# Optimization experiments

Measured on AMD Instinct MI355X. Metric: run time of the kernel, lower is better.

The kernel has to match this reference:

```python
import jax, jax.numpy as jnp
import numpy as np

D_STATE = 8
DT_RANK = 8  # ceil(128/16)


def _grouped_1x1(x, w):
    # x: (B,H,W,Cin), w: (g, Cout//g, Cin//g)
    B, H, W, _ = x.shape
    g, o, i = w.shape
    xg = x.reshape(B, H, W, g, i)
    return jnp.einsum('bhwgi,goi->bhwgo', xg, w).reshape(B, H, W, g * o)


def setup_inputs() -> dict:
    key = jax.random.key(0)
    ks = jax.random.split(key, 16)
    B, H, W, C = 8, 64, 64, 128
    g = 4
    D = 128  # expand_dim = d_inner
    N = D_STATE
    R = DT_RANK
    inp = {}
    inp['x'] = jax.random.normal(ks[0], (B, H, W, C), dtype=jnp.float32)
    inp['w1'] = jax.random.normal(ks[1], (g, D // g, C // g), dtype=jnp.float32) * 0.1
    inp['dw'] = jax.random.normal(ks[2], (3, 3, 1, D), dtype=jnp.float32) * 0.1  # HWIO depthwise
    inp['in_proj_w'] = jax.random.normal(ks[3], (2 * D, D), dtype=jnp.float32) * 0.05
    inp['conv1d_w'] = jax.random.normal(ks[4], (D, 3), dtype=jnp.float32) * 0.1
    inp['conv1d_b'] = jax.random.normal(ks[5], (D,), dtype=jnp.float32) * 0.05
    inp['x_proj_w'] = jax.random.normal(ks[6], (R + 2 * N, D), dtype=jnp.float32) * 0.05
    inp['dt_proj_w'] = jax.random.normal(ks[7], (D, R), dtype=jnp.float32) * 0.05
    inp['dt_proj_b'] = jax.random.normal(ks[8], (D,), dtype=jnp.float32) * 0.05
    inp['A_log'] = jnp.log(jnp.tile(jnp.arange(1, N + 1, dtype=jnp.float32)[None, :], (D, 1)))
    inp['D_param'] = jnp.ones((D,), dtype=jnp.float32)
    inp['out_proj_w'] = jax.random.normal(ks[9], (D, D), dtype=jnp.float32) * 0.05
    inp['gamma'] = jnp.ones((D,), dtype=jnp.float32)
    inp['beta'] = jnp.zeros((D,), dtype=jnp.float32)
    inp['w2'] = jax.random.normal(ks[10], (g, D // g, C // g), dtype=jnp.float32) * 0.1
    inp['wout'] = jax.random.normal(ks[11], (g, C // g, D // g), dtype=jnp.float32) * 0.1
    return inp


def _mamba(x_seq, in_proj_w, conv1d_w, conv1d_b, x_proj_w, dt_proj_w, dt_proj_b, A_log, D_param, out_proj_w):
    # x_seq: (B, L, D)
    B, L, D = x_seq.shape
    N, R = D_STATE, DT_RANK
    xz = jnp.einsum('bld,ed->ble', x_seq, in_proj_w)  # (B,L,2D)
    u, z = xz[..., :D], xz[..., D:]
    # causal depthwise conv1d, kernel=3, left pad 2 (torch: padding=2, slice [:L])
    up = jnp.pad(u, ((0, 0), (2, 0), (0, 0)))
    u = (up[:, 0:L] * conv1d_w[:, 0] + up[:, 1:L + 1] * conv1d_w[:, 1]
         + up[:, 2:L + 2] * conv1d_w[:, 2] + conv1d_b)
    u = jax.nn.silu(u)
    x_dbl = jnp.einsum('bld,ed->ble', u, x_proj_w)  # (B,L,R+2N)
    dt = x_dbl[..., :R]
    Bm = x_dbl[..., R:R + N]
    Cm = x_dbl[..., R + N:]
    delta = jax.nn.softplus(jnp.einsum('blr,dr->bld', dt, dt_proj_w) + dt_proj_b)  # (B,L,D)
    A = -jnp.exp(A_log)  # (D,N)

    def step(h, inp):
        d_t, u_t, b_t, c_t = inp  # (B,D),(B,D),(B,N),(B,N)
        dA = jnp.exp(d_t[..., None] * A)            # (B,D,N)
        h = dA * h + (d_t * u_t)[..., None] * b_t[:, None, :]
        y_t = jnp.einsum('bdn,bn->bd', h, c_t)
        return h, y_t

    h0 = jnp.zeros((B, D, N), dtype=x_seq.dtype)
    xs = (jnp.swapaxes(delta, 0, 1), jnp.swapaxes(u, 0, 1),
          jnp.swapaxes(Bm, 0, 1), jnp.swapaxes(Cm, 0, 1))
    _, ys = jax.lax.scan(step, h0, xs)              # ys: (L,B,D)
    y = jnp.swapaxes(ys, 0, 1) + u * D_param
    y = y * jax.nn.silu(z)
    return jnp.einsum('bld,ed->ble', y, out_proj_w)


def reference(x, w1, dw, in_proj_w, conv1d_w, conv1d_b, x_proj_w, dt_proj_w, dt_proj_b,
              A_log, D_param, out_proj_w, gamma, beta, w2, wout):
    B, H, W, C = x.shape
    D = dw.shape[-1]
    x1 = _grouped_1x1(x, w1)  # (B,H,W,D)
    x1 = jax.lax.conv_general_dilated(
        x1, dw, window_strides=(1, 1), padding='SAME',
        feature_group_count=D, dimension_numbers=('NHWC', 'HWIO', 'NHWC'))
    x1 = jax.nn.silu(x1)
    x1_seq = x1.reshape(B, H * W, D)
    x1_seq = _mamba(x1_seq, in_proj_w, conv1d_w, conv1d_b, x_proj_w,
                    dt_proj_w, dt_proj_b, A_log, D_param, out_proj_w)
    x1 = x1_seq.reshape(B, H, W, D)
    mu = jnp.mean(x1, axis=-1, keepdims=True)
    var = jnp.mean(jnp.square(x1 - mu), axis=-1, keepdims=True)
    x1 = (x1 - mu) * jax.lax.rsqrt(var + 1e-5) * gamma + beta
    x2 = jax.nn.silu(_grouped_1x1(x, w2))
    x_fuse = x1 * x2
    return _grouped_1x1(x_fuse, wout)  # (B,H,W,C)
```

## Files before the change

### kernel.cpp

```cpp
#include <hip/hip_runtime.h>
#include <math.h>

#define B_    8
#define C_    128
#define D_    128
#define L_    4096
#define NPOS_ 32768
#define NC_   128
#define S_    32
#define NB_   4194304
#define MFL_  1048576

typedef __attribute__((ext_vector_type(8))) short short8;
typedef __attribute__((ext_vector_type(4))) float f32x4;

__device__ __forceinline__ float siluf(float x) { return x / (1.f + __expf(-x)); }
__device__ __forceinline__ float softplusf(float x) {
    if (x > 20.f) return x;
    return log1pf(__expf(x));
}
__device__ __forceinline__ unsigned short f2bf(float f) {
    unsigned int u = __float_as_uint(f);
    u = (u + 0x7FFFu + ((u >> 16) & 1u)) >> 16;
    return (unsigned short)u;
}
__device__ __forceinline__ float bf2f(unsigned short h) {
    return __uint_as_float(((unsigned int)h) << 16);
}

__global__ __launch_bounds__(256) void k0_cvt(const float* __restrict__ inW,
                                              const float* __restrict__ OW,
                                              const float* __restrict__ xpw,
                                              unsigned short* __restrict__ inWb,
                                              unsigned short* __restrict__ OWb,
                                              unsigned short* __restrict__ xpwb) {
    for (int i = blockIdx.x * 256 + threadIdx.x; i < 52224; i += gridDim.x * 256) {
        if (i < 32768)      inWb[i] = f2bf(inW[i]);
        else if (i < 49152) OWb[i - 32768] = f2bf(OW[i - 32768]);
        else                xpwb[i - 49152] = f2bf(xpw[i - 49152]);
    }
}

__global__ __launch_bounds__(256) void k1_g1x1(const float* __restrict__ x,
                                               const float* __restrict__ w1,
                                               const float* __restrict__ w2,
                                               float* __restrict__ t1,
                                               float* __restrict__ x2s) {
    __shared__ float xs[16 * 128];
    int t = threadIdx.x;
    int d = t & 127, ph = t >> 7;
    int g = d >> 5, o = d & 31;
    float w1r[32], w2r[32];
    #pragma unroll
    for (int i = 0; i < 32; ++i) {
        w1r[i] = w1[g * 1024 + o * 32 + i];
        w2r[i] = w2[g * 1024 + o * 32 + i];
    }
    int pos0 = blockIdx.x * 64;
    for (int it = 0; it < 4; ++it) {
        int p0 = pos0 + it * 16;
        #pragma unroll
        for (int q = 0; q < 2; ++q) {
            int fi = t * 2 + q;
            *(float4*)&xs[fi * 4] = *(const float4*)&x[p0 * 128 + fi * 4];
        }
        __syncthreads();
        #pragma unroll
        for (int q = 0; q < 8; ++q) {
            int pl = ph * 8 + q;
            float a1 = 0.f, a2 = 0.f;
            const float* xr = &xs[pl * 128 + g * 32];
            #pragma unroll
            for (int i4 = 0; i4 < 8; ++i4) {
                float4 xv = *(const float4*)&xr[i4 * 4];
                a1 += xv.x * w1r[i4*4] + xv.y * w1r[i4*4+1] + xv.z * w1r[i4*4+2] + xv.w * w1r[i4*4+3];
                a2 += xv.x * w2r[i4*4] + xv.y * w2r[i4*4+1] + xv.z * w2r[i4*4+2] + xv.w * w2r[i4*4+3];
            }
            int pos = p0 + pl;
            t1[pos * 128 + d]  = a1;
            x2s[pos * 128 + d] = siluf(a2);
        }
        __syncthreads();
    }
}

__global__ __launch_bounds__(128) void k2_dwconv(const float* __restrict__ t1,
                                                 const float* __restrict__ dw,
                                                 unsigned short* __restrict__ x1cb) {
    int d = threadIdx.x;
    float dwr[9];
    #pragma unroll
    for (int k = 0; k < 9; ++k) dwr[k] = dw[k * 128 + d];
    int bid = blockIdx.x;
    int wt = bid & 7, ht = (bid >> 3) & 7, b = bid >> 6;
    int h0 = ht * 8, w0 = wt * 8;
    float rows[10][10];
    #pragma unroll
    for (int r = 0; r < 10; ++r) {
        int hh = h0 - 1 + r;
        bool hv = (hh >= 0) && (hh < 64);
        #pragma unroll
        for (int c = 0; c < 10; ++c) {
            int w = w0 - 1 + c;
            bool wvv = (w >= 0) && (w < 64);
            rows[r][c] = (hv && wvv) ? t1[((b * 64 + hh) * 64 + w) * 128 + d] : 0.f;
        }
    }
    #pragma unroll
    for (int hi = 0; hi < 8; ++hi) {
        #pragma unroll
        for (int wi = 0; wi < 8; ++wi) {
            float acc = rows[hi][wi]     * dwr[0] + rows[hi][wi+1]   * dwr[1] + rows[hi][wi+2]   * dwr[2]
                      + rows[hi+1][wi]   * dwr[3] + rows[hi+1][wi+1] * dwr[4] + rows[hi+1][wi+2] * dwr[5]
                      + rows[hi+2][wi]   * dwr[6] + rows[hi+2][wi+1] * dwr[7] + rows[hi+2][wi+2] * dwr[8];
            x1cb[((b * 64 + h0 + hi) * 64 + w0 + wi) * 128 + d] = f2bf(siluf(acc));
        }
    }
}

__global__ __launch_bounds__(256) void k3_mfma(const unsigned short* __restrict__ Abf,
                                               const unsigned short* __restrict__ Bbf,
                                               float* __restrict__ uraw,
                                               unsigned short* __restrict__ zb) {
    __shared__ unsigned short Al[128 * 72];
    __shared__ unsigned short Bl[128 * 72];
    int t = threadIdx.x;
    int mtile = blockIdx.x >> 1, ntile = blockIdx.x & 1;
    int pos0 = mtile * 128, n0g = ntile * 128;
    int lane = t & 63, wv = t >> 6;
    int m0 = (wv & 1) * 64, n0w = (wv >> 1) * 64;
    int lanem = lane & 15, laneq = lane >> 4;
    f32x4 acc[4][4];
    #pragma unroll
    for (int i = 0; i < 4; ++i)
        #pragma unroll
        for (int j = 0; j < 4; ++j) acc[i][j] = (f32x4){0.f, 0.f, 0.f, 0.f};
    for (int kc = 0; kc < 2; ++kc) {
        #pragma unroll
        for (int q = 0; q < 4; ++q) {
            int c = t + q * 256;
            int row = c >> 3, col = c & 7;
            *(int4*)&Al[row * 72 + col * 8] = *(const int4*)&Abf[(pos0 + row) * 128 + kc * 64 + col * 8];
            *(int4*)&Bl[row * 72 + col * 8] = *(const int4*)&Bbf[(n0g + row) * 128 + kc * 64 + col * 8];
        }
        __syncthreads();
        #pragma unroll
        for (int ks = 0; ks < 2; ++ks) {
            short8 af[4], bfr[4];
            #pragma unroll
            for (int mi = 0; mi < 4; ++mi)
                af[mi] = *(const short8*)&Al[(m0 + mi * 16 + lanem) * 72 + ks * 32 + laneq * 8];
            #pragma unroll
            for (int ni = 0; ni < 4; ++ni)
                bfr[ni] = *(const short8*)&Bl[(n0w + ni * 16 + lanem) * 72 + ks * 32 + laneq * 8];
            #pragma unroll
            for (int mi = 0; mi < 4; ++mi)
                #pragma unroll
                for (int ni = 0; ni < 4; ++ni)
                    acc[mi][ni] = __builtin_amdgcn_mfma_f32_16x16x32_bf16(af[mi], bfr[ni], acc[mi][ni], 0, 0, 0);
        }
        __syncthreads();
    }
    #pragma unroll
    for (int mi = 0; mi < 4; ++mi)
        #pragma unroll
        for (int ni = 0; ni < 4; ++ni)
            #pragma unroll
            for (int r = 0; r < 4; ++r) {
                int m = pos0 + m0 + mi * 16 + laneq * 4 + r;
                int n = n0w + ni * 16 + lanem;
                if (ntile) zb[m * 128 + n] = f2bf(acc[mi][ni][r]);
                else       uraw[m * 128 + n] = acc[mi][ni][r];
            }
}

__global__ __launch_bounds__(256) void k4_convproj(const float* __restrict__ uraw,
                                                   const float* __restrict__ cw,
                                                   const float* __restrict__ cb,
                                                   const unsigned short* __restrict__ xpwb,
                                                   const float* __restrict__ dtw,
                                                   const float* __restrict__ dtb,
                                                   float* __restrict__ u,
                                                   float* __restrict__ delta,
                                                   float* __restrict__ Bm,
                                                   float* __restrict__ Cm) {
    __shared__ unsigned short uA[64 * 136];
    __shared__ unsigned short xB[32 * 136];
    __shared__ float xdb[64 * 36];
    int t = threadIdx.x;
    int d = t & 127, ph = t >> 7;
    for (int i = t; i < 32 * 128; i += 256) {
        int n = i >> 7, k = i & 127;
        xB[n * 136 + k] = (n < 24) ? xpwb[n * 128 + k] : (unsigned short)0;
    }
    float cw0 = cw[d * 3 + 0], cw1 = cw[d * 3 + 1], cw2 = cw[d * 3 + 2], cbr = cb[d];
    float dtwr[8];
    #pragma unroll
    for (int r = 0; r < 8; ++r) dtwr[r] = dtw[d * 8 + r];
    float dtbr = dtb[d];

    int gpos0 = blockIdx.x * 64;
    int ll0 = (gpos0 & 4095) + ph * 32;
    int base = (gpos0 + ph * 32) * 128 + d;
    float ur0 = (ll0 >= 2) ? uraw[base - 256] : 0.f;
    float ur1 = (ll0 >= 1) ? uraw[base - 128] : 0.f;
    #pragma unroll
    for (int q = 0; q < 32; ++q) {
        float urq = uraw[base + q * 128];
        float us = siluf(ur0 * cw0 + ur1 * cw1 + urq * cw2 + cbr);
        u[base + q * 128] = us;
        uA[(ph * 32 + q) * 136 + d] = f2bf(us);
        ur0 = ur1; ur1 = urq;
    }
    __syncthreads();
    int lane = t & 63, wv = t >> 6;
    int lanem = lane & 15, laneq = lane >> 4;
    f32x4 accx[2];
    accx[0] = (f32x4){0.f, 0.f, 0.f, 0.f};
    accx[1] = (f32x4){0.f, 0.f, 0.f, 0.f};
    #pragma unroll
    for (int ks = 0; ks < 4; ++ks) {
        short8 af = *(const short8*)&uA[(wv * 16 + lanem) * 136 + ks * 32 + laneq * 8];
        #pragma unroll
        for (int nj = 0; nj < 2; ++nj) {
            short8 bfr = *(const short8*)&xB[(nj * 16 + lanem) * 136 + ks * 32 + laneq * 8];
            accx[nj] = __builtin_amdgcn_mfma_f32_16x16x32_bf16(af, bfr, accx[nj], 0, 0, 0);
        }
    }
    #pragma unroll
    for (int nj = 0; nj < 2; ++nj)
        #pragma unroll
        for (int r = 0; r < 4; ++r)
            xdb[(wv * 16 + laneq * 4 + r) * 36 + nj * 16 + lanem] = accx[nj][r];
    __syncthreads();
    #pragma unroll
    for (int q = 0; q < 32; ++q) {
        int pl = ph * 32 + q;
        float dt = dtbr;
        #pragma unroll
        for (int r = 0; r < 8; ++r) dt += xdb[pl * 36 + r] * dtwr[r];
        delta[base + q * 128] = softplusf(dt);
    }
    for (int i = t; i < 1024; i += 256) {
        int p = i >> 4, j = i & 15;
        float v = xdb[p * 36 + 8 + j];
        int gp = gpos0 + p;
        if (j < 8) Bm[gp * 8 + j] = v;
        else       Cm[gp * 8 + (j - 8)] = v;
    }
}

__global__ __launch_bounds__(128) void k5_scan1(const float* __restrict__ delta,
                                                const float* __restrict__ u,
                                                const float* __restrict__ Bm,
                                                const float* __restrict__ A_log,
                                                float* __restrict__ cA,
                                                float* __restrict__ cB) {
    int d = threadIdx.x;
    int bc = blockIdx.x;
    int b = bc >> 7, c = bc & 127;
    float Ar[8];
    #pragma unroll
    for (int n = 0; n < 8; ++n) Ar[n] = -__expf(A_log[d * 8 + n]);
    float h[8], ap[8];
    #pragma unroll
    for (int n = 0; n < 8; ++n) { h[n] = 0.f; ap[n] = 1.f; }
    int base  = (b * L_ + c * S_) * 128 + d;
    int bbase = (b * L_ + c * S_) * 8;
    for (int s = 0; s < S_; ++s) {
        float dl = delta[base + s * 128];
        float uv = u[base + s * 128];
        float du = dl * uv;
        float4 bm0 = *(const float4*)&Bm[bbase + s * 8];
        float4 bm1 = *(const float4*)&Bm[bbase + s * 8 + 4];
        float a;
        a = __expf(dl * Ar[0]); ap[0] *= a; h[0] = a * h[0] + du * bm0.x;
        a = __expf(dl * Ar[1]); ap[1] *= a; h[1] = a * h[1] + du * bm0.y;
        a = __expf(dl * Ar[2]); ap[2] *= a; h[2] = a * h[2] + du * bm0.z;
        a = __expf(dl * Ar[3]); ap[3] *= a; h[3] = a * h[3] + du * bm0.w;
        a = __expf(dl * Ar[4]); ap[4] *= a; h[4] = a * h[4] + du * bm1.x;
        a = __expf(dl * Ar[5]); ap[5] *= a; h[5] = a * h[5] + du * bm1.y;
        a = __expf(dl * Ar[6]); ap[6] *= a; h[6] = a * h[6] + du * bm1.z;
        a = __expf(dl * Ar[7]); ap[7] *= a; h[7] = a * h[7] + du * bm1.w;
    }
    int obase = (bc * 128 + d) * 8;
    *(float4*)&cA[obase]     = make_float4(ap[0], ap[1], ap[2], ap[3]);
    *(float4*)&cA[obase + 4] = make_float4(ap[4], ap[5], ap[6], ap[7]);
    *(float4*)&cB[obase]     = make_float4(h[0], h[1], h[2], h[3]);
    *(float4*)&cB[obase + 4] = make_float4(h[4], h[5], h[6], h[7]);
}

__global__ __launch_bounds__(128) void k6_scan2(const float* __restrict__ cA,
                                                const float* __restrict__ cB,
                                                float* __restrict__ carry) {
    int b = blockIdx.x >> 3;
    int slice = blockIdx.x & 7;
    int dn = slice * 128 + threadIdx.x;
    float h = 0.f;
    for (int c = 0; c < NC_; ++c) {
        int idx = (b * NC_ + c) * 1024 + dn;
        float a  = cA[idx];
        float bv = cB[idx];
        carry[idx] = h;
        h = a * h + bv;
    }
}

__global__ __launch_bounds__(128) void k7_scan3(const float* __restrict__ delta,
                                                const float* __restrict__ u,
                                                const float* __restrict__ Bm,
                                                const float* __restrict__ Cm,
                                                const unsigned short* __restrict__ zb,
                                                const float* __restrict__ A_log,
                                                const float* __restrict__ Dp,
                                                const float* __restrict__ carry,
                                                unsigned short* __restrict__ ybf) {
    int d = threadIdx.x;
    int bc = blockIdx.x;
    int b = bc >> 7, c = bc & 127;
    float Ar[8];
    #pragma unroll
    for (int n = 0; n < 8; ++n) Ar[n] = -__expf(A_log[d * 8 + n]);
    float Dpr = Dp[d];
    int cbase = (bc * 128 + d) * 8;
    float4 h0 = *(const float4*)&carry[cbase];
    float4 h1 = *(const float4*)&carry[cbase + 4];
    float h[8] = {h0.x, h0.y, h0.z, h0.w, h1.x, h1.y, h1.z, h1.w};
    int base  = (b * L_ + c * S_) * 128 + d;
    int bbase = (b * L_ + c * S_) * 8;
    for (int s = 0; s < S_; ++s) {
        float dl = delta[base + s * 128];
        float uv = u[base + s * 128];
        float zv = bf2f(zb[base + s * 128]);
        float du = dl * uv;
        float4 bm0 = *(const float4*)&Bm[bbase + s * 8];
        float4 bm1 = *(const float4*)&Bm[bbase + s * 8 + 4];
        float4 cm0 = *(const float4*)&Cm[bbase + s * 8];
        float4 cm1 = *(const float4*)&Cm[bbase + s * 8 + 4];
        float a;
        a = __expf(dl * Ar[0]); h[0] = a * h[0] + du * bm0.x;
        a = __expf(dl * Ar[1]); h[1] = a * h[1] + du * bm0.y;
        a = __expf(dl * Ar[2]); h[2] = a * h[2] + du * bm0.z;
        a = __expf(dl * Ar[3]); h[3] = a * h[3] + du * bm0.w;
        a = __expf(dl * Ar[4]); h[4] = a * h[4] + du * bm1.x;
        a = __expf(dl * Ar[5]); h[5] = a * h[5] + du * bm1.y;
        a = __expf(dl * Ar[6]); h[6] = a * h[6] + du * bm1.z;
        a = __expf(dl * Ar[7]); h[7] = a * h[7] + du * bm1.w;
        float yv = h[0] * cm0.x + h[1] * cm0.y + h[2] * cm0.z + h[3] * cm0.w
                 + h[4] * cm1.x + h[5] * cm1.y + h[6] * cm1.z + h[7] * cm1.w;
        yv = (yv + uv * Dpr) * siluf(zv);
        ybf[base + s * 128] = f2bf(yv);
    }
}

__global__ __launch_bounds__(256) void k8a_mfma(const unsigned short* __restrict__ Abf,
                                                const unsigned short* __restrict__ Bbf,
                                                float* __restrict__ xz) {
    __shared__ unsigned short Al[128 * 72];
    __shared__ unsigned short Bl[128 * 72];
    int t = threadIdx.x;
    int pos0 = blockIdx.x * 128;
    int lane = t & 63, wv = t >> 6;
    int m0 = (wv & 1) * 64, n0w = (wv >> 1) * 64;
    int lanem = lane & 15, laneq = lane >> 4;
    f32x4 acc[4][4];
    #pragma unroll
    for (int i = 0; i < 4; ++i)
        #pragma unroll
        for (int j = 0; j < 4; ++j) acc[i][j] = (f32x4){0.f, 0.f, 0.f, 0.f};
    for (int kc = 0; kc < 2; ++kc) {
        #pragma unroll
        for (int q = 0; q < 4; ++q) {
            int c = t + q * 256;
            int row = c >> 3, col = c & 7;
            *(int4*)&Al[row * 72 + col * 8] = *(const int4*)&Abf[(pos0 + row) * 128 + kc * 64 + col * 8];
            *(int4*)&Bl[row * 72 + col * 8] = *(const int4*)&Bbf[row * 128 + kc * 64 + col * 8];
        }
        __syncthreads();
        #pragma unroll
        for (int ks = 0; ks < 2; ++ks) {
            short8 af[4], bfr[4];
            #pragma unroll
            for (int mi = 0; mi < 4; ++mi)
                af[mi] = *(const short8*)&Al[(m0 + mi * 16 + lanem) * 72 + ks * 32 + laneq * 8];
            #pragma unroll
            for (int ni = 0; ni < 4; ++ni)
                bfr[ni] = *(const short8*)&Bl[(n0w + ni * 16 + lanem) * 72 + ks * 32 + laneq * 8];
            #pragma unroll
            for (int mi = 0; mi < 4; ++mi)
                #pragma unroll
                for (int ni = 0; ni < 4; ++ni)
                    acc[mi][ni] = __builtin_amdgcn_mfma_f32_16x16x32_bf16(af[mi], bfr[ni], acc[mi][ni], 0, 0, 0);
        }
        __syncthreads();
    }
    #pragma unroll
    for (int mi = 0; mi < 4; ++mi)
        #pragma unroll
        for (int ni = 0; ni < 4; ++ni)
            #pragma unroll
            for (int r = 0; r < 4; ++r) {
                int m = pos0 + m0 + mi * 16 + laneq * 4 + r;
                int n = n0w + ni * 16 + lanem;
                xz[m * 128 + n] = acc[mi][ni][r];
            }
}

__global__ __launch_bounds__(256) void k8b_epi(const float* __restrict__ xz,
                                               const float* __restrict__ gamma,
                                               const float* __restrict__ beta,
                                               const float* __restrict__ x2s,
                                               const float* __restrict__ wout,
                                               float* __restrict__ out) {
    __shared__ float wt[32 * 128];
    __shared__ float xfs[32 * 132];
    int t  = threadIdx.x;
    int te = t & 31, tp = t >> 5;
    for (int idx = t; idx < 4096; idx += 256) {
        int i = idx >> 7, c = idx & 127;
        wt[idx] = wout[(c >> 5) * 1024 + (c & 31) * 32 + i];
    }
    float gr[4], br[4];
    #pragma unroll
    for (int j = 0; j < 4; ++j) { gr[j] = gamma[te + 32 * j]; br[j] = beta[te + 32 * j]; }

    int pos0 = blockIdx.x * 32;
    float acc[4][4];
    #pragma unroll
    for (int i = 0; i < 4; ++i) {
        int pos = pos0 + tp * 4 + i;
        #pragma unroll
        for (int j = 0; j < 4; ++j) acc[i][j] = xz[pos * 128 + te + 32 * j];
    }
    #pragma unroll
    for (int i = 0; i < 4; ++i) {
        float s  = acc[i][0] + acc[i][1] + acc[i][2] + acc[i][3];
        float s2 = acc[i][0]*acc[i][0] + acc[i][1]*acc[i][1] + acc[i][2]*acc[i][2] + acc[i][3]*acc[i][3];
        #pragma unroll
        for (int off = 16; off >= 1; off >>= 1) {
            s  += __shfl_xor(s, off, 64);
            s2 += __shfl_xor(s2, off, 64);
        }
        float m = s * (1.f / 128.f);
        float var = s2 * (1.f / 128.f) - m * m;
        float rstd = rsqrtf(var + 1e-5f);
        int pos = pos0 + tp * 4 + i;
        #pragma unroll
        for (int j = 0; j < 4; ++j) {
            int e = te + 32 * j;
            float v = (acc[i][j] - m) * rstd * gr[j] + br[j];
            v *= x2s[pos * 128 + e];
            xfs[(tp * 4 + i) * 132 + e] = v;
        }
    }
    __syncthreads();
    #pragma unroll
    for (int i = 0; i < 4; ++i) {
        int pos = pos0 + tp * 4 + i;
        const float* xr = &xfs[(tp * 4 + i) * 132];
        float a2[4] = {0.f, 0.f, 0.f, 0.f};
        for (int ii = 0; ii < 32; ++ii) {
            #pragma unroll
            for (int j = 0; j < 4; ++j)
                a2[j] += xr[j * 32 + ii] * wt[ii * 128 + 32 * j + te];
        }
        #pragma unroll
        for (int j = 0; j < 4; ++j) out[pos * 128 + 32 * j + te] = a2[j];
    }
}

extern "C" void kernel_launch(void* const* d_in, const int* in_sizes, int n_in,
                              void* d_out, int out_size, void* d_ws, size_t ws_size,
                              hipStream_t stream) {
    (void)in_sizes; (void)n_in; (void)out_size; (void)ws_size;
    const float* x         = (const float*)d_in[0];
    const float* w1        = (const float*)d_in[1];
    const float* dw        = (const float*)d_in[2];
    const float* in_proj_w = (const float*)d_in[3];
    const float* conv1d_w  = (const float*)d_in[4];
    const float* conv1d_b  = (const float*)d_in[5];
    const float* x_proj_w  = (const float*)d_in[6];
    const float* dt_proj_w = (const float*)d_in[7];
    const float* dt_proj_b = (const float*)d_in[8];
    const float* A_log     = (const float*)d_in[9];
    const float* D_param   = (const float*)d_in[10];
    const float* out_proj_w= (const float*)d_in[11];
    const float* gamma     = (const float*)d_in[12];
    const float* beta      = (const float*)d_in[13];
    const float* w2        = (const float*)d_in[14];
    const float* wout      = (const float*)d_in[15];
    float* out = (float*)d_out;

    float* ws = (float*)d_ws;
    float* t1    = ws;
    float* x2s   = ws + 4 * (size_t)MFL_;
    float* uraw  = ws + 8 * (size_t)MFL_;
    unsigned short* zb = (unsigned short*)(ws + 12 * (size_t)MFL_);
    float* delta = ws + 16 * (size_t)MFL_;
    unsigned short* x1cb = (unsigned short*)(ws + 16 * (size_t)MFL_);
    unsigned short* ybf  = (unsigned short*)(ws + 20 * (size_t)MFL_);
    float* Bm    = ws + 22 * (size_t)MFL_;
    float* Cm    = Bm + (size_t)NPOS_ * 8;
    float* cA    = Cm + (size_t)NPOS_ * 8;
    float* cB    = cA + (size_t)MFL_;
    float* carry = cB + (size_t)MFL_;
    unsigned short* inWb = (unsigned short*)(carry + (size_t)MFL_);
    unsigned short* OWb  = inWb + 32768;
    unsigned short* xpwb = OWb + 16384;
    float* u  = t1;
    float* xz = uraw;

    k0_cvt<<<64, 256, 0, stream>>>(in_proj_w, out_proj_w, x_proj_w, inWb, OWb, xpwb);
    k1_g1x1<<<512, 256, 0, stream>>>(x, w1, w2, t1, x2s);
    k2_dwconv<<<512, 128, 0, stream>>>(t1, dw, x1cb);
    k3_mfma<<<512, 256, 0, stream>>>(x1cb, inWb, uraw, zb);
    k4_convproj<<<512, 256, 0, stream>>>(uraw, conv1d_w, conv1d_b, xpwb,
                                         dt_proj_w, dt_proj_b, u, delta, Bm, Cm);
    k5_scan1<<<1024, 128, 0, stream>>>(delta, u, Bm, A_log, cA, cB);
    k6_scan2<<<64, 128, 0, stream>>>(cA, cB, carry);
    k7_scan3<<<1024, 128, 0, stream>>>(delta, u, Bm, Cm, zb, A_log, D_param, carry, ybf);
    k8a_mfma<<<256, 256, 0, stream>>>(ybf, OWb, xz);
    k8b_epi<<<1024, 256, 0, stream>>>(xz, gamma, beta, x2s, wout, out);
}
```

Before: 250.9 us.

## Fuse scan pass 1 into conv/proj kernel, recompute u and delta, store intermediates as bf16

The first chunked-scan pass is folded into the conv1d/x_proj kernel, so delta and u are no longer written to memory. The third scan pass recomputes u and delta from the bf16 raw projection and a packed 24-float x_proj buffer. Several fp32 intermediates (t1, x2s, uraw, the out_proj result) are now stored as bf16, roughly halving memory traffic between kernels. The cost is extra transcendental work in pass 3 and lower precision in the intermediates.

```diff
diff --git a/kernel.cpp b/kernel.cpp
--- a/kernel.cpp
+++ b/kernel.cpp
@@ -8,7 +8,6 @@
 #define NPOS_ 32768
 #define NC_   128
 #define S_    32
-#define NB_   4194304
 #define MFL_  1048576
 
 typedef __attribute__((ext_vector_type(8))) short short8;
@@ -44,8 +43,8 @@
 __global__ __launch_bounds__(256) void k1_g1x1(const float* __restrict__ x,
                                                const float* __restrict__ w1,
                                                const float* __restrict__ w2,
-                                               float* __restrict__ t1,
-                                               float* __restrict__ x2s) {
+                                               unsigned short* __restrict__ t1b,
+                                               unsigned short* __restrict__ x2sb) {
     __shared__ float xs[16 * 128];
     int t = threadIdx.x;
     int d = t & 127, ph = t >> 7;
@@ -77,14 +76,14 @@
                 a2 += xv.x * w2r[i4*4] + xv.y * w2r[i4*4+1] + xv.z * w2r[i4*4+2] + xv.w * w2r[i4*4+3];
             }
             int pos = p0 + pl;
-            t1[pos * 128 + d]  = a1;
-            x2s[pos * 128 + d] = siluf(a2);
+            t1b[pos * 128 + d]  = f2bf(a1);
+            x2sb[pos * 128 + d] = f2bf(siluf(a2));
         }
         __syncthreads();
     }
 }
 
-__global__ __launch_bounds__(128) void k2_dwconv(const float* __restrict__ t1,
+__global__ __launch_bounds__(128) void k2_dwconv(const unsigned short* __restrict__ t1b,
                                                  const float* __restrict__ dw,
                                                  unsigned short* __restrict__ x1cb) {
     int d = threadIdx.x;
@@ -103,7 +102,7 @@
         for (int c = 0; c < 10; ++c) {
             int w = w0 - 1 + c;
             bool wvv = (w >= 0) && (w < 64);
-            rows[r][c] = (hv && wvv) ? t1[((b * 64 + hh) * 64 + w) * 128 + d] : 0.f;
+            rows[r][c] = (hv && wvv) ? bf2f(t1b[((b * 64 + hh) * 64 + w) * 128 + d]) : 0.f;
         }
     }
     #pragma unroll
@@ -120,7 +119,7 @@
 
 __global__ __launch_bounds__(256) void k3_mfma(const unsigned short* __restrict__ Abf,
                                                const unsigned short* __restrict__ Bbf,
-                                               float* __restrict__ uraw,
+                                               unsigned short* __restrict__ urawb,
                                                unsigned short* __restrict__ zb) {
     __shared__ unsigned short Al[128 * 72];
     __shared__ unsigned short Bl[128 * 72];
@@ -161,6 +160,7 @@
         }
         __syncthreads();
     }
+    unsigned short* dst = ntile ? zb : urawb;
     #pragma unroll
     for (int mi = 0; mi < 4; ++mi)
         #pragma unroll
@@ -169,21 +169,20 @@
             for (int r = 0; r < 4; ++r) {
                 int m = pos0 + m0 + mi * 16 + laneq * 4 + r;
                 int n = n0w + ni * 16 + lanem;
-                if (ntile) zb[m * 128 + n] = f2bf(acc[mi][ni][r]);
-                else       uraw[m * 128 + n] = acc[mi][ni][r];
+                dst[m * 128 + n] = f2bf(acc[mi][ni][r]);
             }
 }
 
-__global__ __launch_bounds__(256) void k4_convproj(const float* __restrict__ uraw,
-                                                   const float* __restrict__ cw,
-                                                   const float* __restrict__ cb,
-                                                   const unsigned short* __restrict__ xpwb,
-                                                   const float* __restrict__ dtw,
-                                                   const float* __restrict__ dtb,
-                                                   float* __restrict__ u,
-                                                   float* __restrict__ delta,
-                                                   float* __restrict__ Bm,
-                                                   float* __restrict__ Cm) {
+__global__ __launch_bounds__(256) void k45_convscan(const unsigned short* __restrict__ urawb,
+                                                    const float* __restrict__ cw,
+                                                    const float* __restrict__ cb,
+                                                    const unsigned short* __restrict__ xpwb,
+                                                    const float* __restrict__ dtw,
+                                                    const float* __restrict__ dtb,
+                                                    const float* __restrict__ A_log,
+                                                    float* __restrict__ xdb24,
+                                                    float* __restrict__ cA,
+                                                    float* __restrict__ cB) {
     __shared__ unsigned short uA[64 * 136];
     __shared__ unsigned short xB[32 * 136];
     __shared__ float xdb[64 * 36];
@@ -198,18 +197,22 @@
     #pragma unroll
     for (int r = 0; r < 8; ++r) dtwr[r] = dtw[d * 8 + r];
     float dtbr = dtb[d];
+    float Ar[8];
+    #pragma unroll
+    for (int n = 0; n < 8; ++n) Ar[n] = -__expf(A_log[d * 8 + n]);
 
     int gpos0 = blockIdx.x * 64;
     int ll0 = (gpos0 & 4095) + ph * 32;
     int base = (gpos0 + ph * 32) * 128 + d;
-    float ur0 = (ll0 >= 2) ? uraw[base - 256] : 0.f;
-    float ur1 = (ll0 >= 1) ? uraw[base - 128] : 0.f;
+    float ur0 = (ll0 >= 2) ? bf2f(urawb[base - 256]) : 0.f;
+    float ur1 = (ll0 >= 1) ? bf2f(urawb[base - 128]) : 0.f;
+    float us[32];
     #pragma unroll
     for (int q = 0; q < 32; ++q) {
-        float urq = uraw[base + q * 128];
-        float us = siluf(ur0 * cw0 + ur1 * cw1 + urq * cw2 + cbr);
-        u[base + q * 128] = us;
-        uA[(ph * 32 + q) * 136 + d] = f2bf(us);
+        float urq = bf2f(urawb[base + q * 128]);
+        float v = siluf(ur0 * cw0 + ur1 * cw1 + urq * cw2 + cbr);
+        us[q] = v;
+        uA[(ph * 32 + q) * 136 + d] = f2bf(v);
         ur0 = ur1; ur1 = urq;
     }
     __syncthreads();
@@ -233,61 +236,35 @@
         for (int r = 0; r < 4; ++r)
             xdb[(wv * 16 + laneq * 4 + r) * 36 + nj * 16 + lanem] = accx[nj][r];
     __syncthreads();
+    float h[8], ap[8];
+    #pragma unroll
+    for (int n = 0; n < 8; ++n) { h[n] = 0.f; ap[n] = 1.f; }
     #pragma unroll
     for (int q = 0; q < 32; ++q) {
         int pl = ph * 32 + q;
         float dt = dtbr;
         #pragma unroll
         for (int r = 0; r < 8; ++r) dt += xdb[pl * 36 + r] * dtwr[r];
-        delta[base + q * 128] = softplusf(dt);
-    }
-    for (int i = t; i < 1024; i += 256) {
-        int p = i >> 4, j = i & 15;
-        float v = xdb[p * 36 + 8 + j];
-        int gp = gpos0 + p;
-        if (j < 8) Bm[gp * 8 + j] = v;
-        else       Cm[gp * 8 + (j - 8)] = v;
-    }
-}
-
-__global__ __launch_bounds__(128) void k5_scan1(const float* __restrict__ delta,
-                                                const float* __restrict__ u,
-                                                const float* __restrict__ Bm,
-                                                const float* __restrict__ A_log,
-                                                float* __restrict__ cA,
-                                                float* __restrict__ cB) {
-    int d = threadIdx.x;
-    int bc = blockIdx.x;
-    int b = bc >> 7, c = bc & 127;
-    float Ar[8];
-    #pragma unroll
-    for (int n = 0; n < 8; ++n) Ar[n] = -__expf(A_log[d * 8 + n]);
-    float h[8], ap[8];
-    #pragma unroll
-    for (int n = 0; n < 8; ++n) { h[n] = 0.f; ap[n] = 1.f; }
-    int base  = (b * L_ + c * S_) * 128 + d;
-    int bbase = (b * L_ + c * S_) * 8;
-    for (int s = 0; s < S_; ++s) {
-        float dl = delta[base + s * 128];
-        float uv = u[base + s * 128];
-        float du = dl * uv;
-        float4 bm0 = *(const float4*)&Bm[bbase + s * 8];
-        float4 bm1 = *(const float4*)&Bm[bbase + s * 8 + 4];
-        float a;
-        a = __expf(dl * Ar[0]); ap[0] *= a; h[0] = a * h[0] + du * bm0.x;
-        a = __expf(dl * Ar[1]); ap[1] *= a; h[1] = a * h[1] + du * bm0.y;
-        a = __expf(dl * Ar[2]); ap[2] *= a; h[2] = a * h[2] + du * bm0.z;
-        a = __expf(dl * Ar[3]); ap[3] *= a; h[3] = a * h[3] + du * bm0.w;
-        a = __expf(dl * Ar[4]); ap[4] *= a; h[4] = a * h[4] + du * bm1.x;
-        a = __expf(dl * Ar[5]); ap[5] *= a; h[5] = a * h[5] + du * bm1.y;
-        a = __expf(dl * Ar[6]); ap[6] *= a; h[6] = a * h[6] + du * bm1.z;
-        a = __expf(dl * Ar[7]); ap[7] *= a; h[7] = a * h[7] + du * bm1.w;
-    }
-    int obase = (bc * 128 + d) * 8;
+        float dl = softplusf(dt);
+        float du = dl * us[q];
+        #pragma unroll
+        for (int n = 0; n < 8; ++n) {
+            float a = __expf(dl * Ar[n]);
+            ap[n] *= a;
+            h[n] = a * h[n] + du * xdb[pl * 36 + 8 + n];
+        }
+    }
+    int bH = gpos0 >> 12;
+    int c  = ((gpos0 & 4095) >> 5) + ph;
+    int obase = ((bH * 128 + c) * 128 + d) * 8;
     *(float4*)&cA[obase]     = make_float4(ap[0], ap[1], ap[2], ap[3]);
     *(float4*)&cA[obase + 4] = make_float4(ap[4], ap[5], ap[6], ap[7]);
     *(float4*)&cB[obase]     = make_float4(h[0], h[1], h[2], h[3]);
     *(float4*)&cB[obase + 4] = make_float4(h[4], h[5], h[6], h[7]);
+    for (int i = t; i < 64 * 24; i += 256) {
+        int p = i / 24, j = i - p * 24;
+        xdb24[(gpos0 + p) * 24 + j] = xdb[p * 36 + j];
+    }
 }
 
 __global__ __launch_bounds__(128) void k6_scan2(const float* __restrict__ cA,
@@ -306,10 +283,12 @@
     }
 }
 
-__global__ __launch_bounds__(128) void k7_scan3(const float* __restrict__ delta,
-                                                const float* __restrict__ u,
-                                                const float* __restrict__ Bm,
-                                                const float* __restrict__ Cm,
+__global__ __launch_bounds__(128) void k7_scan3(const unsigned short* __restrict__ urawb,
+                                                const float* __restrict__ cw,
+                                                const float* __restrict__ cb,
+                                                const float* __restrict__ dtw,
+                                                const float* __restrict__ dtb,
+                                                const float* __restrict__ xdb24,
                                                 const unsigned short* __restrict__ zb,
                                                 const float* __restrict__ A_log,
                                                 const float* __restrict__ Dp,
@@ -322,21 +301,35 @@
     #pragma unroll
     for (int n = 0; n < 8; ++n) Ar[n] = -__expf(A_log[d * 8 + n]);
     float Dpr = Dp[d];
+    float cw0 = cw[d * 3 + 0], cw1 = cw[d * 3 + 1], cw2 = cw[d * 3 + 2], cbr = cb[d];
+    float dtwr[8];
+    #pragma unroll
+    for (int r = 0; r < 8; ++r) dtwr[r] = dtw[d * 8 + r];
+    float dtbr = dtb[d];
     int cbase = (bc * 128 + d) * 8;
     float4 h0 = *(const float4*)&carry[cbase];
     float4 h1 = *(const float4*)&carry[cbase + 4];
     float h[8] = {h0.x, h0.y, h0.z, h0.w, h1.x, h1.y, h1.z, h1.w};
-    int base  = (b * L_ + c * S_) * 128 + d;
-    int bbase = (b * L_ + c * S_) * 8;
+    int l0 = c * S_;
+    int base  = (b * L_ + l0) * 128 + d;
+    int xbase = (b * L_ + l0) * 24;
+    float ur0 = (l0 >= 2) ? bf2f(urawb[base - 256]) : 0.f;
+    float ur1 = (l0 >= 1) ? bf2f(urawb[base - 128]) : 0.f;
     for (int s = 0; s < S_; ++s) {
-        float dl = delta[base + s * 128];
-        float uv = u[base + s * 128];
+        float urq = bf2f(urawb[base + s * 128]);
+        float uv = siluf(ur0 * cw0 + ur1 * cw1 + urq * cw2 + cbr);
+        ur0 = ur1; ur1 = urq;
+        float4 dt0 = *(const float4*)&xdb24[xbase + s * 24];
+        float4 dt1 = *(const float4*)&xdb24[xbase + s * 24 + 4];
+        float4 bm0 = *(const float4*)&xdb24[xbase + s * 24 + 8];
+        float4 bm1 = *(const float4*)&xdb24[xbase + s * 24 + 12];
+        float4 cm0 = *(const float4*)&xdb24[xbase + s * 24 + 16];
+        float4 cm1 = *(const float4*)&xdb24[xbase + s * 24 + 20];
+        float dt = dtbr + dt0.x * dtwr[0] + dt0.y * dtwr[1] + dt0.z * dtwr[2] + dt0.w * dtwr[3]
+                        + dt1.x * dtwr[4] + dt1.y * dtwr[5] + dt1.z * dtwr[6] + dt1.w * dtwr[7];
+        float dl = softplusf(dt);
         float zv = bf2f(zb[base + s * 128]);
         float du = dl * uv;
-        float4 bm0 = *(const float4*)&Bm[bbase + s * 8];
-        float4 bm1 = *(const float4*)&Bm[bbase + s * 8 + 4];
-        float4 cm0 = *(const float4*)&Cm[bbase + s * 8];
-        float4 cm1 = *(const float4*)&Cm[bbase + s * 8 + 4];
         float a;
         a = __expf(dl * Ar[0]); h[0] = a * h[0] + du * bm0.x;
         a = __expf(dl * Ar[1]); h[1] = a * h[1] + du * bm0.y;
@@ -355,7 +348,7 @@
 
 __global__ __launch_bounds__(256) void k8a_mfma(const unsigned short* __restrict__ Abf,
                                                 const unsigned short* __restrict__ Bbf,
-                                                float* __restrict__ xz) {
+                                                unsigned short* __restrict__ xzb) {
     __shared__ unsigned short Al[128 * 72];
     __shared__ unsigned short Bl[128 * 72];
     int t = threadIdx.x;
@@ -402,14 +395,14 @@
             for (int r = 0; r < 4; ++r) {
                 int m = pos0 + m0 + mi * 16 + laneq * 4 + r;
                 int n = n0w + ni * 16 + lanem;
-                xz[m * 128 + n] = acc[mi][ni][r];
+                xzb[m * 128 + n] = f2bf(acc[mi][ni][r]);
             }
 }
 
-__global__ __launch_bounds__(256) void k8b_epi(const float* __restrict__ xz,
+__global__ __launch_bounds__(256) void k8b_epi(const unsigned short* __restrict__ xzb,
                                                const float* __restrict__ gamma,
                                                const float* __restrict__ beta,
-                                               const float* __restrict__ x2s,
+                                               const unsigned short* __restrict__ x2sb,
                                                const float* __restrict__ wout,
                                                float* __restrict__ out) {
     __shared__ float wt[32 * 128];
@@ -430,7 +423,7 @@
     for (int i = 0; i < 4; ++i) {
         int pos = pos0 + tp * 4 + i;
         #pragma unroll
-        for (int j = 0; j < 4; ++j) acc[i][j] = xz[pos * 128 + te + 32 * j];
+        for (int j = 0; j < 4; ++j) acc[i][j] = bf2f(xzb[pos * 128 + te + 32 * j]);
     }
     #pragma unroll
     for (int i = 0; i < 4; ++i) {
@@ -449,7 +442,7 @@
         for (int j = 0; j < 4; ++j) {
             int e = te + 32 * j;
             float v = (acc[i][j] - m) * rstd * gr[j] + br[j];
-            v *= x2s[pos * 128 + e];
+            v *= bf2f(x2sb[pos * 128 + e]);
             xfs[(tp * 4 + i) * 132 + e] = v;
         }
     }
@@ -492,33 +485,31 @@
     float* out = (float*)d_out;
 
     float* ws = (float*)d_ws;
-    float* t1    = ws;
-    float* x2s   = ws + 4 * (size_t)MFL_;
-    float* uraw  = ws + 8 * (size_t)MFL_;
-    unsigned short* zb = (unsigned short*)(ws + 12 * (size_t)MFL_);
-    float* delta = ws + 16 * (size_t)MFL_;
-    unsigned short* x1cb = (unsigned short*)(ws + 16 * (size_t)MFL_);
-    unsigned short* ybf  = (unsigned short*)(ws + 20 * (size_t)MFL_);
-    float* Bm    = ws + 22 * (size_t)MFL_;
-    float* Cm    = Bm + (size_t)NPOS_ * 8;
-    float* cA    = Cm + (size_t)NPOS_ * 8;
+    unsigned short* x2sb  = (unsigned short*)(ws);
+    unsigned short* t1b   = (unsigned short*)(ws + 2  * (size_t)MFL_);
+    unsigned short* x1cb  = (unsigned short*)(ws + 4  * (size_t)MFL_);
+    unsigned short* urawb = (unsigned short*)(ws + 6  * (size_t)MFL_);
+    unsigned short* zb    = (unsigned short*)(ws + 8  * (size_t)MFL_);
+    unsigned short* ybf   = (unsigned short*)(ws + 10 * (size_t)MFL_);
+    unsigned short* xzb   = (unsigned short*)(ws + 12 * (size_t)MFL_);
+    float* xdb24 = ws + 14 * (size_t)MFL_;
+    float* cA    = xdb24 + (size_t)NPOS_ * 24;
     float* cB    = cA + (size_t)MFL_;
     float* carry = cB + (size_t)MFL_;
     unsigned short* inWb = (unsigned short*)(carry + (size_t)MFL_);
     unsigned short* OWb  = inWb + 32768;
     unsigned short* xpwb = OWb + 16384;
-    float* u  = t1;
-    float* xz = uraw;
 
     k0_cvt<<<64, 256, 0, stream>>>(in_proj_w, out_proj_w, x_proj_w, inWb, OWb, xpwb);
-    k1_g1x1<<<512, 256, 0, stream>>>(x, w1, w2, t1, x2s);
-    k2_dwconv<<<512, 128, 0, stream>>>(t1, dw, x1cb);
-    k3_mfma<<<512, 256, 0, stream>>>(x1cb, inWb, uraw, zb);
-    k4_convproj<<<512, 256, 0, stream>>>(uraw, conv1d_w, conv1d_b, xpwb,
-                                         dt_proj_w, dt_proj_b, u, delta, Bm, Cm);
-    k5_scan1<<<1024, 128, 0, stream>>>(delta, u, Bm, A_log, cA, cB);
+    k1_g1x1<<<512, 256, 0, stream>>>(x, w1, w2, t1b, x2sb);
+    k2_dwconv<<<512, 128, 0, stream>>>(t1b, dw, x1cb);
+    k3_mfma<<<512, 256, 0, stream>>>(x1cb, inWb, urawb, zb);
+    k45_convscan<<<512, 256, 0, stream>>>(urawb, conv1d_w, conv1d_b, xpwb,
+                                          dt_proj_w, dt_proj_b, A_log,
+                                          xdb24, cA, cB);
     k6_scan2<<<64, 128, 0, stream>>>(cA, cB, carry);
-    k7_scan3<<<1024, 128, 0, stream>>>(delta, u, Bm, Cm, zb, A_log, D_param, carry, ybf);
-    k8a_mfma<<<256, 256, 0, stream>>>(ybf, OWb, xz);
-    k8b_epi<<<1024, 256, 0, stream>>>(xz, gamma, beta, x2s, wout, out);
-}
+    k7_scan3<<<1024, 128, 0, stream>>>(urawb, conv1d_w, conv1d_b, dt_proj_w, dt_proj_b,
+                                       xdb24, zb, A_log, D_param, carry, ybf);
+    k8a_mfma<<<256, 256, 0, stream>>>(ybf, OWb, xzb);
+    k8b_epi<<<1024, 256, 0, stream>>>(xzb, gamma, beta, x2sb, wout, out);
+}
```

New measurement: 285.8 us. +13.9%, slower.
